# Kernel tuning notes

Measured on AMD Instinct MI355X. Metric: run time of the kernel, lower is better.

Reference implementation:

```python
import jax, jax.numpy as jnp
import numpy as np


def _conv(x, w, b, stride, pad):
    # x: NCHW, w: OIHW
    y = jax.lax.conv_general_dilated(
        x, w, window_strides=(stride, stride),
        padding=[(pad, pad), (pad, pad)],
        dimension_numbers=('NCHW', 'OIHW', 'NCHW'))
    return y + b[None, :, None, None]


def setup_inputs() -> dict:
    key = jax.random.key(0)
    ks = jax.random.split(key, 12)
    W = 0.05  # weight init scale
    emb_max = float(np.sqrt(3.0 / 512))  # matches nn.init.uniform_(-max, max)
    return {
        'x':    jax.random.normal(ks[0], (64, 1, 256, 256), jnp.float32),
        'w1':   jax.random.normal(ks[1], (64, 1, 4, 4), jnp.float32) * W,
        'b1':   jnp.zeros((64,), jnp.float32),
        'w2':   jax.random.normal(ks[2], (128, 64, 4, 4), jnp.float32) * W,
        'b2':   jnp.zeros((128,), jnp.float32),
        'w3':   jax.random.normal(ks[3], (128, 128, 3, 3), jnp.float32) * W,
        'b3':   jnp.zeros((128,), jnp.float32),
        'r1w1': jax.random.normal(ks[4], (32, 128, 3, 3), jnp.float32) * W,
        'r1b1': jnp.zeros((32,), jnp.float32),
        'r1w2': jax.random.normal(ks[5], (128, 32, 1, 1), jnp.float32) * W,
        'r1b2': jnp.zeros((128,), jnp.float32),
        'r2w1': jax.random.normal(ks[6], (32, 128, 3, 3), jnp.float32) * W,
        'r2b1': jnp.zeros((32,), jnp.float32),
        'r2w2': jax.random.normal(ks[7], (128, 32, 1, 1), jnp.float32) * W,
        'r2b2': jnp.zeros((128,), jnp.float32),
        'w4':   jax.random.normal(ks[8], (64, 128, 1, 1), jnp.float32) * W,
        'b4':   jnp.zeros((64,), jnp.float32),
        'emb':  jax.random.uniform(ks[9], (512, 64), jnp.float32, -emb_max, emb_max),
    }


def _residual(h, rw1, rb1, rw2, rb2):
    # x + Conv1x1(ReLU(Conv3x3(ReLU(x))))
    t = _conv(jax.nn.relu(h), rw1, rb1, 1, 1)
    t = _conv(jax.nn.relu(t), rw2, rb2, 1, 0)
    return h + t


def reference(x, w1, b1, w2, b2, w3, b3,
              r1w1, r1b1, r1w2, r1b2, r2w1, r2b1, r2w2, r2b2,
              w4, b4, emb):
    # --- Encoder ---
    h = jax.nn.relu(_conv(x, w1, b1, 2, 1))   # (B,64,128,128)
    h = jax.nn.relu(_conv(h, w2, b2, 2, 1))   # (B,128,64,64)
    h = _conv(h, w3, b3, 1, 1)                # (B,128,64,64)
    h = _residual(h, r1w1, r1b1, r1w2, r1b2)
    h = _residual(h, r2w1, r2b1, r2w2, r2b2)
    h = jax.nn.relu(h)
    z = _conv(h, w4, b4, 1, 0)                # (B,64,64,64) = (B,D,H,W)

    # --- VectorQuantisizer ---
    z = jnp.moveaxis(z, 1, -1)                # (B,H,W,D)
    B, H, Wd, D = z.shape
    flat = z.reshape(-1, D)                   # (N,D)
    d = (jnp.sum(flat * flat, axis=-1, keepdims=True)
         - 2.0 * flat @ emb.T
         + jnp.sum(emb * emb, axis=-1)[None, :])   # (N,512)
    idx = jnp.argmin(d, axis=-1)              # (N,)
    # one_hot.float() @ emb  ==  gather rows
    quantized = emb[idx].reshape(B, H, Wd, D)
    return quantized
```

## Files before the change

kernel.cpp:

```cpp
#include <hip/hip_runtime.h>

#define TDIM 16

typedef unsigned short u16;
typedef __attribute__((ext_vector_type(8))) short bf16x8;
typedef __attribute__((ext_vector_type(4))) float f32x4;

__device__ __forceinline__ float b2f(u16 u) {
  return __uint_as_float(((unsigned)u) << 16);
}
__device__ __forceinline__ u16 f2bf(float f) {
  unsigned u = __float_as_uint(f);
  unsigned r = 0x7FFFu + ((u >> 16) & 1u);
  return (u16)((u + r) >> 16);
}

template<int OC>
__global__ __launch_bounds__(256) void repack_k(const float* __restrict__ w,
                                                float* __restrict__ wT, int tot) {
  int i = blockIdx.x * 256 + threadIdx.x;
  if (i >= tot) return;
  int row = i / OC, oc = i - row * OC;
  wT[i] = w[(size_t)oc * (size_t)(tot / OC) + row];
}

template<int OC, int IC>
__global__ __launch_bounds__(256) void repack_mf3(const float* __restrict__ w,
                                                  short* __restrict__ hi,
                                                  short* __restrict__ mid,
                                                  short* __restrict__ lo) {
  constexpr int NCH = IC / 32;
  int tot = OC * IC * 9;
  int i = blockIdx.x * 256 + threadIdx.x;
  if (i >= tot) return;
  int icl = i & 31;
  int rem = i >> 5;
  int oc = rem % OC; rem /= OC;
  int ch = rem % NCH;
  int pos = rem / NCH;
  int ic = ch * 32 + icl;
  int ky = pos / 3, kx = pos - ky * 3;
  float v = w[((size_t)(oc * IC + ic) * 3 + ky) * 3 + kx];
  u16 h = f2bf(v);
  float t1 = v - b2f(h);
  u16 m = f2bf(t1);
  float t2 = t1 - b2f(m);
  hi[i] = (short)h;
  mid[i] = (short)m;
  lo[i] = (short)f2bf(t2);
}

__global__ __launch_bounds__(256) void e2_k(const float* __restrict__ emb,
                                            float* __restrict__ e2) {
  int r = blockIdx.x * 256 + threadIdx.x;
  if (r >= 512) return;
  float s = 0.f;
#pragma unroll
  for (int d = 0; d < 64; ++d) s = fmaf(emb[r * 64 + d], emb[r * 64 + d], s);
  e2[r] = s;
}

template<int MT, bool RELU_IN>
__global__ __launch_bounds__(256, 2) void conv_mf3(
    const float* __restrict__ in, const short* __restrict__ wh,
    const short* __restrict__ wm, const short* __restrict__ wl,
    const float* __restrict__ bias, float* __restrict__ out) {
  constexpr int OC = MT * 16;
  __shared__ __align__(16) short xh[10560];
  __shared__ __align__(16) short xm[10560];
  __shared__ __align__(16) short xl[10560];

  const int tid = threadIdx.x;
  const int n = blockIdx.y;
  const int r0 = blockIdx.x * 2;
  const int wv = tid >> 6, lane = tid & 63;
  const int nlo = lane & 15, kg = lane >> 4;

  f32x4 acc[MT][2];
#pragma unroll
  for (int mt = 0; mt < MT; ++mt)
#pragma unroll
    for (int ti = 0; ti < 2; ++ti) acc[mt][ti] = (f32x4){0.f, 0.f, 0.f, 0.f};

#pragma unroll 1
  for (int ch = 0; ch < 4; ++ch) {
    __syncthreads();
    for (int i = tid; i < 8448; i += 256) {
      int c = i % 66;
      int rem = i / 66;
      int lr = rem & 3, icl = rem >> 2;
      int gr = r0 - 1 + lr, gc = c - 1;
      float v = 0.f;
      if (gr >= 0 && gr < 64 && gc >= 0 && gc < 64)
        v = in[((size_t)(n * 128 + ch * 32 + icl) * 64 + gr) * 64 + gc];
      if (RELU_IN) v = fmaxf(v, 0.f);
      u16 h = f2bf(v);
      float t1 = v - b2f(h);
      u16 m = f2bf(t1);
      float t2 = t1 - b2f(m);
      int a = (lr * 66 + c) * 40 + icl;
      xh[a] = (short)h;
      xm[a] = (short)m;
      xl[a] = (short)f2bf(t2);
    }
    __syncthreads();

#pragma unroll 1
    for (int pos = 0; pos < 9; ++pos) {
      const int ky = pos / 3, kx = pos - ky * 3;
      bf16x8 bh[2], bm[2], bl[2];
#pragma unroll
      for (int ti = 0; ti < 2; ++ti) {
        int t = wv * 2 + ti;
        int lr = (t >> 2) + ky;
        int c = (t & 3) * 16 + nlo + kx;
        int a = (lr * 66 + c) * 40 + kg * 8;
        bh[ti] = *(const bf16x8*)(xh + a);
        bm[ti] = *(const bf16x8*)(xm + a);
        bl[ti] = *(const bf16x8*)(xl + a);
      }
      const size_t wo =
          ((size_t)(pos * 4 + ch) * OC + nlo) * 32 + (size_t)kg * 8;
#pragma unroll
      for (int mt = 0; mt < MT; ++mt) {
        const size_t o = wo + (size_t)mt * 16 * 32;
        bf16x8 AH = *(const bf16x8*)(wh + o);
        bf16x8 AM = *(const bf16x8*)(wm + o);
        bf16x8 AL = *(const bf16x8*)(wl + o);
#pragma unroll
        for (int ti = 0; ti < 2; ++ti) {
          acc[mt][ti] = __builtin_amdgcn_mfma_f32_16x16x32_bf16(
              AH, bh[ti], acc[mt][ti], 0, 0, 0);
          acc[mt][ti] = __builtin_amdgcn_mfma_f32_16x16x32_bf16(
              AH, bm[ti], acc[mt][ti], 0, 0, 0);
          acc[mt][ti] = __builtin_amdgcn_mfma_f32_16x16x32_bf16(
              AM, bh[ti], acc[mt][ti], 0, 0, 0);
          acc[mt][ti] = __builtin_amdgcn_mfma_f32_16x16x32_bf16(
              AH, bl[ti], acc[mt][ti], 0, 0, 0);
          acc[mt][ti] = __builtin_amdgcn_mfma_f32_16x16x32_bf16(
              AL, bh[ti], acc[mt][ti], 0, 0, 0);
          acc[mt][ti] = __builtin_amdgcn_mfma_f32_16x16x32_bf16(
              AM, bm[ti], acc[mt][ti], 0, 0, 0);
        }
      }
    }
  }

#pragma unroll
  for (int mt = 0; mt < MT; ++mt)
#pragma unroll
    for (int ti = 0; ti < 2; ++ti) {
      int t = wv * 2 + ti;
      int grow = r0 + (t >> 2);
      int px = (t & 3) * 16 + nlo;
#pragma unroll
      for (int j = 0; j < 4; ++j) {
        int oc = mt * 16 + kg * 4 + j;
        out[((size_t)(n * OC + oc) * 64 + grow) * 64 + px] =
            acc[mt][ti][j] + bias[oc];
      }
    }
}

template<int IC, int OC, int K, int S, int PAD, int CCH, int IH, int IW,
         bool RELU_IN, bool RELU_OUT>
__global__ __launch_bounds__(256) void conv_direct(
    const float* __restrict__ in, const float* __restrict__ wT,
    const float* __restrict__ bias, float* __restrict__ out) {
  constexpr int OH = (IH + 2 * PAD - K) / S + 1;
  constexpr int OW = OH;
  constexpr int RS = (TDIM - 1) * S + K;
  constexpr int CS = RS;
  constexpr int TX = OW / TDIM;
  constexpr int TOT = CCH * RS * CS;
  constexpr int WSLAB = CCH * K * K * OC;

  __shared__ __align__(16) float lds[TOT];
  __shared__ __align__(16) float wlds[WSLAB];

  const int tid = threadIdx.x;
  const int n = blockIdx.y;
  const int tile = blockIdx.x;
  const int oh0 = (tile / TX) * TDIM;
  const int ow0 = (tile % TX) * TDIM;
  const int ty = tid >> 4, tx = tid & 15;
  const int oh = oh0 + ty, ow = ow0 + tx;

  float acc[OC];
#pragma unroll
  for (int oc = 0; oc < OC; ++oc) acc[oc] = bias[oc];

  for (int ic0 = 0; ic0 < IC; ic0 += CCH) {
    __syncthreads();
    for (int i = tid; i < TOT; i += 256) {
      int c = i / (RS * CS);
      int rem = i - c * (RS * CS);
      int r = rem / CS;
      int col = rem - r * CS;
      int gr = oh0 * S + r - PAD;
      int gc = ow0 * S + col - PAD;
      float v = 0.f;
      if (gr >= 0 && gr < IH && gc >= 0 && gc < IW) {
        v = in[((size_t)(n * IC + ic0 + c) * IH + gr) * IW + gc];
        if (RELU_IN) v = fmaxf(v, 0.f);
      }
      lds[i] = v;
    }
    {
      const float* wsrc = wT + (size_t)ic0 * (K * K * OC);
      for (int i = tid; i < WSLAB; i += 256) wlds[i] = wsrc[i];
    }
    __syncthreads();
#pragma unroll 1
    for (int c = 0; c < CCH; ++c) {
#pragma unroll
      for (int ky = 0; ky < K; ++ky)
#pragma unroll
        for (int kx = 0; kx < K; ++kx) {
          float v = lds[(c * RS + ty * S + ky) * CS + tx * S + kx];
          const float4* w4 =
              (const float4*)(wlds + (c * K * K + ky * K + kx) * OC);
#pragma unroll
          for (int q = 0; q < OC / 4; ++q) {
            float4 wv = w4[q];
            acc[4 * q + 0] = fmaf(wv.x, v, acc[4 * q + 0]);
            acc[4 * q + 1] = fmaf(wv.y, v, acc[4 * q + 1]);
            acc[4 * q + 2] = fmaf(wv.z, v, acc[4 * q + 2]);
            acc[4 * q + 3] = fmaf(wv.w, v, acc[4 * q + 3]);
          }
        }
    }
  }

#pragma unroll
  for (int oc = 0; oc < OC; ++oc) {
    float r = acc[oc];
    if (RELU_OUT) r = fmaxf(r, 0.f);
    out[((size_t)(n * OC + oc) * OH + oh) * OW + ow] = r;
  }
}

template<int IC, int OC>
__global__ __launch_bounds__(256) void conv1x1_res(
    const float* __restrict__ in, const float* __restrict__ wT,
    const float* __restrict__ bias, const float* __restrict__ res,
    float* __restrict__ out) {
  __shared__ __align__(16) float wlds[IC * OC];
  for (int i = threadIdx.x; i < IC * OC; i += 256) wlds[i] = wT[i];
  __syncthreads();

  const int pid = blockIdx.x * 256 + threadIdx.x;
  const int n = pid >> 12, px = pid & 4095;
  const float* ip = in + (size_t)n * IC * 4096 + px;
  float acc[OC];
#pragma unroll
  for (int o = 0; o < OC; ++o) acc[o] = bias[o];
#pragma unroll 4
  for (int i = 0; i < IC; ++i) {
    float v = fmaxf(ip[(size_t)i * 4096], 0.f);
    const float4* w4 = (const float4*)(wlds + i * OC);
#pragma unroll
    for (int q = 0; q < OC / 4; ++q) {
      float4 wv = w4[q];
      acc[4 * q + 0] = fmaf(wv.x, v, acc[4 * q + 0]);
      acc[4 * q + 1] = fmaf(wv.y, v, acc[4 * q + 1]);
      acc[4 * q + 2] = fmaf(wv.z, v, acc[4 * q + 2]);
      acc[4 * q + 3] = fmaf(wv.w, v, acc[4 * q + 3]);
    }
  }
  const float* rp = res + (size_t)n * OC * 4096 + px;
  float* op = out + (size_t)n * OC * 4096 + px;
#pragma unroll
  for (int o = 0; o < OC; ++o) op[(size_t)o * 4096] = rp[(size_t)o * 4096] + acc[o];
}

__global__ __launch_bounds__(256) void conv4_vq(
    const float* __restrict__ h, const float* __restrict__ wT4,
    const float* __restrict__ b4, const float* __restrict__ emb,
    const float* __restrict__ e2, float* __restrict__ out) {
  __shared__ __align__(16) float wlds[128 * 64];
  __shared__ __align__(16) float elds[64 * 64];
  __shared__ float e2lds[512];

  const int tid = threadIdx.x;
  for (int i = tid; i < 128 * 64; i += 256) wlds[i] = wT4[i];
  for (int i = tid; i < 512; i += 256) e2lds[i] = e2[i];
  __syncthreads();

  const int pid = blockIdx.x * 256 + tid;
  const int n = pid >> 12, px = pid & 4095;
  const float* ip = h + (size_t)n * 128 * 4096 + px;
  float z[64];
#pragma unroll
  for (int d = 0; d < 64; ++d) z[d] = b4[d];
#pragma unroll 2
  for (int i = 0; i < 128; ++i) {
    float v = fmaxf(ip[(size_t)i * 4096], 0.f);
    const float4* w4 = (const float4*)(wlds + i * 64);
#pragma unroll
    for (int q = 0; q < 16; ++q) {
      float4 wv = w4[q];
      z[4 * q + 0] = fmaf(wv.x, v, z[4 * q + 0]);
      z[4 * q + 1] = fmaf(wv.y, v, z[4 * q + 1]);
      z[4 * q + 2] = fmaf(wv.z, v, z[4 * q + 2]);
      z[4 * q + 3] = fmaf(wv.w, v, z[4 * q + 3]);
    }
  }
  float z2 = 0.f;
#pragma unroll
  for (int d = 0; d < 64; ++d) z2 = fmaf(z[d], z[d], z2);

  float best = __builtin_inff();
  int bidx = 0;
  for (int r0 = 0; r0 < 512; r0 += 64) {
    __syncthreads();
    for (int i = tid; i < 64 * 64; i += 256) elds[i] = emb[(size_t)r0 * 64 + i];
    __syncthreads();
#pragma unroll 1
    for (int r = 0; r < 64; ++r) {
      const float4* e4 = (const float4*)(elds + r * 64);
      float p0 = 0.f, p1 = 0.f, p2 = 0.f, p3 = 0.f;
#pragma unroll
      for (int q = 0; q < 16; ++q) {
        float4 ev = e4[q];
        p0 = fmaf(ev.x, z[4 * q + 0], p0);
        p1 = fmaf(ev.y, z[4 * q + 1], p1);
        p2 = fmaf(ev.z, z[4 * q + 2], p2);
        p3 = fmaf(ev.w, z[4 * q + 3], p3);
      }
      float dot = (p0 + p1) + (p2 + p3);
      float dist = (z2 - 2.f * dot) + e2lds[r0 + r];
      if (dist < best) { best = dist; bidx = r0 + r; }
    }
  }

  const float4* eb = (const float4*)(emb + (size_t)bidx * 64);
  float4* op = (float4*)(out + (size_t)pid * 64);
#pragma unroll
  for (int q = 0; q < 16; ++q) op[q] = eb[q];
}

extern "C" void kernel_launch(void* const* d_in, const int* in_sizes, int n_in,
                              void* d_out, int out_size, void* d_ws, size_t ws_size,
                              hipStream_t stream) {
  const float* x    = (const float*)d_in[0];
  const float* w1   = (const float*)d_in[1];
  const float* b1   = (const float*)d_in[2];
  const float* w2   = (const float*)d_in[3];
  const float* b2   = (const float*)d_in[4];
  const float* w3   = (const float*)d_in[5];
  const float* b3   = (const float*)d_in[6];
  const float* r1w1 = (const float*)d_in[7];
  const float* r1b1 = (const float*)d_in[8];
  const float* r1w2 = (const float*)d_in[9];
  const float* r1b2 = (const float*)d_in[10];
  const float* r2w1 = (const float*)d_in[11];
  const float* r2b1 = (const float*)d_in[12];
  const float* r2w2 = (const float*)d_in[13];
  const float* r2b2 = (const float*)d_in[14];
  const float* w4   = (const float*)d_in[15];
  const float* b4   = (const float*)d_in[16];
  const float* emb  = (const float*)d_in[17];

  char* ws = (char*)d_ws;
  float* wT1   = (float*)ws;
  float* wT2   = wT1 + 1024;
  float* wTr1b = wT2 + 131072;
  float* wTr2b = wTr1b + 4096;
  float* wT4   = wTr2b + 4096;
  float* e2v   = wT4 + 8192;
  short* c3h   = (short*)(e2v + 512);
  short* c3m   = c3h + 147456;
  short* c3l   = c3m + 147456;
  short* r1h   = c3l + 147456;
  short* r1m   = r1h + 36864;
  short* r1l   = r1m + 36864;
  short* r2h   = r1l + 36864;
  short* r2m   = r2h + 36864;
  short* r2l   = r2m + 36864;

  const size_t WOFF = 3ull << 20;
  const size_t SZ_A = 4194304ull;
  const size_t SZ_B = 2097152ull;
  const size_t SZ_C = 524288ull;
  const size_t PER_IMG = SZ_A + SZ_B + SZ_C;
  int NB = 64;
  while (NB > 1 && WOFF + (size_t)NB * PER_IMG > ws_size) NB >>= 1;

  char* bufs = ws + WOFF;
  float* A  = (float*)bufs;
  float* B_ = (float*)(bufs + (size_t)NB * SZ_A);
  float* C_ = (float*)(bufs + (size_t)NB * (SZ_A + SZ_B));

  auto blk = [](int tot) { return (tot + 255) / 256; };
  repack_k<64> <<<blk(1024),   256, 0, stream>>>(w1,   wT1,   1024);
  repack_k<128><<<blk(131072), 256, 0, stream>>>(w2,   wT2,   131072);
  repack_k<128><<<blk(4096),   256, 0, stream>>>(r1w2, wTr1b, 4096);
  repack_k<128><<<blk(4096),   256, 0, stream>>>(r2w2, wTr2b, 4096);
  repack_k<64> <<<blk(8192),   256, 0, stream>>>(w4,   wT4,   8192);
  repack_mf3<128, 128><<<blk(147456), 256, 0, stream>>>(w3, c3h, c3m, c3l);
  repack_mf3<32, 128> <<<blk(36864),  256, 0, stream>>>(r1w1, r1h, r1m, r1l);
  repack_mf3<32, 128> <<<blk(36864),  256, 0, stream>>>(r2w1, r2h, r2m, r2l);
  e2_k<<<2, 256, 0, stream>>>(emb, e2v);

  for (int n0 = 0; n0 < 64; n0 += NB) {
    const int nb = (64 - n0 < NB) ? (64 - n0) : NB;
    const float* xc = x + (size_t)n0 * 65536;
    float* oc = (float*)d_out + (size_t)n0 * 4096 * 64;

    conv_direct<1, 64, 4, 2, 1, 1, 256, 256, false, true>
        <<<dim3(64, nb), 256, 0, stream>>>(xc, wT1, b1, A);
    conv_direct<64, 128, 4, 2, 1, 4, 128, 128, false, true>
        <<<dim3(16, nb), 256, 0, stream>>>(A, wT2, b2, B_);
    conv_mf3<8, false><<<dim3(32, nb), 256, 0, stream>>>(
        B_, c3h, c3m, c3l, b3, A);
    conv_mf3<2, true><<<dim3(32, nb), 256, 0, stream>>>(
        A, r1h, r1m, r1l, r1b1, C_);
    conv1x1_res<32, 128><<<nb * 16, 256, 0, stream>>>(C_, wTr1b, r1b2, A, B_);
    conv_mf3<2, true><<<dim3(32, nb), 256, 0, stream>>>(
        B_, r2h, r2m, r2l, r2b1, C_);
    conv1x1_res<32, 128><<<nb * 16, 256, 0, stream>>>(C_, wTr2b, r2b2, B_, A);
    conv4_vq<<<nb * 16, 256, 0, stream>>>(A, wT4, b4, emb, e2v, oc);
  }
}
```

Baseline: 3.307 ms.

## Move stride-2 4x4 conv2 from scalar FP32 to split-bf16 MFMA kernel

Replaces the FP32 direct convolution for the second encoder layer with an MFMA kernel. The kernel splits both weights and activations into three bf16 terms (hi/mid/lo) and accumulates six cross products to keep near-FP32 accuracy. A new repack kernel lays out the w2 weights in the split format, indexed by ky and input-channel chunk. The intent is to move the most FLOP-heavy early conv onto matrix cores. The cost is six MFMAs per product, plus per-tile conversion work and LDS traffic for the stride-2 input tile.

```diff
diff --git a/kernel.cpp b/kernel.cpp
--- a/kernel.cpp
+++ b/kernel.cpp
@@ -50,6 +50,28 @@
   lo[i] = (short)f2bf(t2);
 }
 
+__global__ __launch_bounds__(256) void repack_mf2(const float* __restrict__ w,
+                                                  short* __restrict__ hi,
+                                                  short* __restrict__ mid,
+                                                  short* __restrict__ lo) {
+  int i = blockIdx.x * 256 + threadIdx.x;
+  if (i >= 131072) return;
+  int icl = i & 7;
+  int kx = (i >> 3) & 3;
+  int oc = (i >> 5) & 127;
+  int t = i >> 12;
+  int ch = t & 7, ky = t >> 3;
+  int ic = ch * 8 + icl;
+  float v = w[((size_t)(oc * 64 + ic) * 4 + ky) * 4 + kx];
+  u16 h = f2bf(v);
+  float t1 = v - b2f(h);
+  u16 m = f2bf(t1);
+  float t2 = t1 - b2f(m);
+  hi[i] = (short)h;
+  mid[i] = (short)m;
+  lo[i] = (short)f2bf(t2);
+}
+
 __global__ __launch_bounds__(256) void e2_k(const float* __restrict__ emb,
                                             float* __restrict__ e2) {
   int r = blockIdx.x * 256 + threadIdx.x;
@@ -158,6 +180,105 @@
         int oc = mt * 16 + kg * 4 + j;
         out[((size_t)(n * OC + oc) * 64 + grow) * 64 + px] =
             acc[mt][ti][j] + bias[oc];
+      }
+    }
+}
+
+__global__ __launch_bounds__(256, 2) void conv_mf2(
+    const float* __restrict__ in, const short* __restrict__ wh,
+    const short* __restrict__ wm, const short* __restrict__ wl,
+    const float* __restrict__ bias, float* __restrict__ out) {
+  __shared__ __align__(16) short xh[6336];
+  __shared__ __align__(16) short xm[6336];
+  __shared__ __align__(16) short xl[6336];
+
+  const int tid = threadIdx.x;
+  const int n = blockIdx.y;
+  const int r0 = blockIdx.x * 2;
+  const int wv = tid >> 6, lane = tid & 63;
+  const int nlo = lane & 15, kg = lane >> 4;
+
+  f32x4 acc[8][2];
+#pragma unroll
+  for (int mt = 0; mt < 8; ++mt)
+#pragma unroll
+    for (int ti = 0; ti < 2; ++ti) acc[mt][ti] = (f32x4){0.f, 0.f, 0.f, 0.f};
+
+#pragma unroll 1
+  for (int ch = 0; ch < 8; ++ch) {
+    __syncthreads();
+    for (int i = tid; i < 6336; i += 256) {
+      int c = i % 132;
+      int rem = i / 132;
+      int lr = rem % 6, icl = rem / 6;
+      int gr = 2 * r0 - 1 + lr, gc = c - 1;
+      float v = 0.f;
+      if (gr >= 0 && gr < 128 && gc >= 0 && gc < 128)
+        v = in[((size_t)(n * 64 + ch * 8 + icl) * 128 + gr) * 128 + gc];
+      u16 h = f2bf(v);
+      float t1 = v - b2f(h);
+      u16 m = f2bf(t1);
+      float t2 = t1 - b2f(m);
+      int a = (lr * 132 + c) * 8 + icl;
+      xh[a] = (short)h;
+      xm[a] = (short)m;
+      xl[a] = (short)f2bf(t2);
+    }
+    __syncthreads();
+
+#pragma unroll 1
+    for (int ky = 0; ky < 4; ++ky) {
+      bf16x8 bh[2], bm[2], bl[2];
+#pragma unroll
+      for (int ti = 0; ti < 2; ++ti) {
+        int t = wv * 2 + ti;
+        int lr = 2 * (t >> 2) + ky;
+        int px = (t & 3) * 16 + nlo;
+        int cidx = 2 * px + kg;
+        int a = (lr * 132 + cidx) * 8;
+        bh[ti] = *(const bf16x8*)(xh + a);
+        bm[ti] = *(const bf16x8*)(xm + a);
+        bl[ti] = *(const bf16x8*)(xl + a);
+      }
+      const size_t wo = ((size_t)(ky * 8 + ch) * 128 + nlo) * 32 +
+                        (size_t)kg * 8;
+#pragma unroll
+      for (int mt = 0; mt < 8; ++mt) {
+        const size_t o = wo + (size_t)mt * 16 * 32;
+        bf16x8 AH = *(const bf16x8*)(wh + o);
+        bf16x8 AM = *(const bf16x8*)(wm + o);
+        bf16x8 AL = *(const bf16x8*)(wl + o);
+#pragma unroll
+        for (int ti = 0; ti < 2; ++ti) {
+          acc[mt][ti] = __builtin_amdgcn_mfma_f32_16x16x32_bf16(
+              AH, bh[ti], acc[mt][ti], 0, 0, 0);
+          acc[mt][ti] = __builtin_amdgcn_mfma_f32_16x16x32_bf16(
+              AH, bm[ti], acc[mt][ti], 0, 0, 0);
+          acc[mt][ti] = __builtin_amdgcn_mfma_f32_16x16x32_bf16(
+              AM, bh[ti], acc[mt][ti], 0, 0, 0);
+          acc[mt][ti] = __builtin_amdgcn_mfma_f32_16x16x32_bf16(
+              AH, bl[ti], acc[mt][ti], 0, 0, 0);
+          acc[mt][ti] = __builtin_amdgcn_mfma_f32_16x16x32_bf16(
+              AL, bh[ti], acc[mt][ti], 0, 0, 0);
+          acc[mt][ti] = __builtin_amdgcn_mfma_f32_16x16x32_bf16(
+              AM, bm[ti], acc[mt][ti], 0, 0, 0);
+        }
+      }
+    }
+  }
+
+#pragma unroll
+  for (int mt = 0; mt < 8; ++mt)
+#pragma unroll
+    for (int ti = 0; ti < 2; ++ti) {
+      int t = wv * 2 + ti;
+      int grow = r0 + (t >> 2);
+      int px = (t & 3) * 16 + nlo;
+#pragma unroll
+      for (int j = 0; j < 4; ++j) {
+        int oc = mt * 16 + kg * 4 + j;
+        out[((size_t)(n * 128 + oc) * 64 + grow) * 64 + px] =
+            fmaxf(acc[mt][ti][j] + bias[oc], 0.f);
       }
     }
 }
@@ -364,8 +485,7 @@
 
   char* ws = (char*)d_ws;
   float* wT1   = (float*)ws;
-  float* wT2   = wT1 + 1024;
-  float* wTr1b = wT2 + 131072;
+  float* wTr1b = wT1 + 1024;
   float* wTr2b = wTr1b + 4096;
   float* wT4   = wTr2b + 4096;
   float* e2v   = wT4 + 8192;
@@ -378,6 +498,9 @@
   short* r2h   = r1l + 36864;
   short* r2m   = r2h + 36864;
   short* r2l   = r2m + 36864;
+  short* w2h   = r2l + 36864;
+  short* w2m   = w2h + 131072;
+  short* w2l   = w2m + 131072;
 
   const size_t WOFF = 3ull << 20;
   const size_t SZ_A = 4194304ull;
@@ -394,10 +517,10 @@
 
   auto blk = [](int tot) { return (tot + 255) / 256; };
   repack_k<64> <<<blk(1024),   256, 0, stream>>>(w1,   wT1,   1024);
-  repack_k<128><<<blk(131072), 256, 0, stream>>>(w2,   wT2,   131072);
   repack_k<128><<<blk(4096),   256, 0, stream>>>(r1w2, wTr1b, 4096);
   repack_k<128><<<blk(4096),   256, 0, stream>>>(r2w2, wTr2b, 4096);
   repack_k<64> <<<blk(8192),   256, 0, stream>>>(w4,   wT4,   8192);
+  repack_mf2<<<blk(131072), 256, 0, stream>>>(w2, w2h, w2m, w2l);
   repack_mf3<128, 128><<<blk(147456), 256, 0, stream>>>(w3, c3h, c3m, c3l);
   repack_mf3<32, 128> <<<blk(36864),  256, 0, stream>>>(r1w1, r1h, r1m, r1l);
   repack_mf3<32, 128> <<<blk(36864),  256, 0, stream>>>(r2w1, r2h, r2m, r2l);
@@ -410,8 +533,7 @@
 
     conv_direct<1, 64, 4, 2, 1, 1, 256, 256, false, true>
         <<<dim3(64, nb), 256, 0, stream>>>(xc, wT1, b1, A);
-    conv_direct<64, 128, 4, 2, 1, 4, 128, 128, false, true>
-        <<<dim3(16, nb), 256, 0, stream>>>(A, wT2, b2, B_);
+    conv_mf2<<<dim3(32, nb), 256, 0, stream>>>(A, w2h, w2m, w2l, b2, B_);
     conv_mf3<8, false><<<dim3(32, nb), 256, 0, stream>>>(
         B_, c3h, c3m, c3l, b3, A);
     conv_mf3<2, true><<<dim3(32, nb), 256, 0, stream>>>(
```

Result: faster. 3.142 ms (-5.0%).
